# Optimization experiments

Hardware: AMD Instinct MI355X
Metric: run time of the kernel (lower is better)

Reference implementation:

```python
import jax, jax.numpy as jnp
import numpy as np

N_HEAD = 16


def setup_inputs() -> dict:
    key = jax.random.key(0)
    k1, k2, k3 = jax.random.split(key, 3)
    B, T, C = 4, 2048, 1024
    x = jax.random.normal(k1, (B, T, C), dtype=jnp.float32)
    Wqkv = jax.random.normal(k2, (C, 3 * C), dtype=jnp.float32) * 0.02
    Wproj = jax.random.normal(k3, (C, C), dtype=jnp.float32) * 0.02
    return {"x": x, "Wqkv": Wqkv, "Wproj": Wproj}


def reference(x, Wqkv, Wproj):
    B, T, C = x.shape
    nh = N_HEAD
    hd = C // nh
    qkv = x @ Wqkv                                  # (B, T, 3C)
    q, k, v = jnp.split(qkv, 3, axis=-1)
    # (B, T, C) -> (B, nh, T, hd)
    q = q.reshape(B, T, nh, hd).transpose(0, 2, 1, 3)
    k = k.reshape(B, T, nh, hd).transpose(0, 2, 1, 3)
    v = v.reshape(B, T, nh, hd).transpose(0, 2, 1, 3)
    # scaled dot-product attention with causal mask (past_kv=None => T_all == T)
    att = jnp.einsum("bhtd,bhsd->bhts", q, k) / jnp.sqrt(jnp.float32(hd))
    causal = jnp.tril(jnp.ones((T, T), dtype=bool))  # (T, T)
    att = jnp.where(causal[None, None, :, :], att, jnp.float32(-jnp.inf))
    att = jax.nn.softmax(att, axis=-1)              # (B, nh, T, T)
    y = jnp.einsum("bhts,bhsd->bhtd", att, v)       # (B, nh, T, hd)
    y = y.transpose(0, 2, 1, 3).reshape(B, T, C)
    y = y @ Wproj                                   # (B, T, C)
    # present_kv (detached in original)
    return y, jax.lax.stop_gradient(k), jax.lax.stop_gradient(v)
```

## Files before the change

kernel.cpp:

```cpp
#include <hip/hip_runtime.h>
#include <hip/hip_bf16.h>


typedef __bf16 bf16;
typedef __attribute__((ext_vector_type(8))) __bf16 bf16x8;
typedef __attribute__((ext_vector_type(4))) __bf16 bf16x4;
typedef __attribute__((ext_vector_type(4))) float f32x4;

#define AS_G __attribute__((address_space(1)))
#define AS_L __attribute__((address_space(3)))

#define QSCALE 0.1803368801111204f

__device__ __forceinline__ void gld_lds16(const bf16* g, bf16* l) {
  __builtin_amdgcn_global_load_lds((const AS_G void*)g, (AS_L void*)l, 16, 0, 0);
}

__global__ __launch_bounds__(256) void k_cast(const float* __restrict__ in,
                                              bf16* __restrict__ out, int n) {
  int i = (blockIdx.x * 256 + threadIdx.x) * 8;
  if (i >= n) return;
  float4 a = *(const float4*)(in + i);
  float4 b = *(const float4*)(in + i + 4);
  bf16x8 o;
  o[0] = (bf16)a.x; o[1] = (bf16)a.y; o[2] = (bf16)a.z; o[3] = (bf16)a.w;
  o[4] = (bf16)b.x; o[5] = (bf16)b.y; o[6] = (bf16)b.z; o[7] = (bf16)b.w;
  *(bf16x8*)(out + i) = o;
}

__global__ __launch_bounds__(256) void k_transpose(const float* __restrict__ in,
                                                   bf16* __restrict__ out,
                                                   int K, int N) {
  __shared__ float tile[32][33];
  int bx = blockIdx.x * 32;
  int by = blockIdx.y * 32;
  int tx = threadIdx.x, ty = threadIdx.y;
#pragma unroll
  for (int i = 0; i < 4; ++i)
    tile[ty + i * 8][tx] = in[(size_t)(by + ty + i * 8) * N + bx + tx];
  __syncthreads();
#pragma unroll
  for (int i = 0; i < 4; ++i)
    out[(size_t)(bx + ty + i * 8) * K + by + tx] = (bf16)tile[tx][ty + i * 8];
}

__device__ __forceinline__ void gemm_tile_128(const bf16* __restrict__ A,
                                              const bf16* __restrict__ Bt,
                                              int m0, int n0,
                                              bf16* As, bf16* Bs,
                                              f32x4 acc[4][4]) {
  const int tid = threadIdx.x;
  const int w = tid >> 6, lane = tid & 63, lo = lane & 15, hi = lane >> 4;
  const int wm = w >> 1, wn = w & 1;
#pragma unroll 1
  for (int k0 = 0; k0 < 1024; k0 += 32) {
#pragma unroll
    for (int p = 0; p < 2; ++p) {
      int u = tid + 256 * p;
      int row = u >> 2, cs = u & 3;
      int g = cs ^ ((row >> 1) & 3);
      gld_lds16(A + (size_t)(m0 + row) * 1024 + k0 + g * 8, As + p * 2048 + w * 512);
      gld_lds16(Bt + (size_t)(n0 + row) * 1024 + k0 + g * 8, Bs + p * 2048 + w * 512);
    }
    __syncthreads();
    bf16x8 af[4], bfr[4];
#pragma unroll
    for (int i = 0; i < 4; ++i) {
      int row = wm * 64 + i * 16 + lo;
      af[i] = *(const bf16x8*)(As + row * 32 + (hi ^ ((row >> 1) & 3)) * 8);
    }
#pragma unroll
    for (int j = 0; j < 4; ++j) {
      int row = wn * 64 + j * 16 + lo;
      bfr[j] = *(const bf16x8*)(Bs + row * 32 + (hi ^ ((row >> 1) & 3)) * 8);
    }
#pragma unroll
    for (int i = 0; i < 4; ++i)
#pragma unroll
      for (int j = 0; j < 4; ++j)
        acc[i][j] = __builtin_amdgcn_mfma_f32_16x16x32_bf16(af[i], bfr[j], acc[i][j], 0, 0, 0);
    __syncthreads();
  }
}

__global__ __launch_bounds__(256) void k_gemm_qkv(const bf16* __restrict__ x,
                                                  const bf16* __restrict__ WqkvT,
                                                  bf16* __restrict__ qb, bf16* __restrict__ kb,
                                                  bf16* __restrict__ vtb,
                                                  float* __restrict__ outk, float* __restrict__ outv) {
  __shared__ bf16 As[128 * 32], Bs[128 * 32];
  f32x4 acc[4][4] = {};
  int m0 = blockIdx.y * 128, n0 = blockIdx.x * 128;
  gemm_tile_128(x, WqkvT, m0, n0, As, Bs, acc);
  const int tid = threadIdx.x;
  const int w = tid >> 6, lane = tid & 63, lo = lane & 15, hi = lane >> 4;
  const int wm = w >> 1, wn = w & 1;
#pragma unroll
  for (int i = 0; i < 4; ++i) {
    int growbase = m0 + wm * 64 + i * 16 + hi * 4;
    int b = growbase >> 11, t0 = growbase & 2047;
#pragma unroll
    for (int j = 0; j < 4; ++j) {
      int gcol = n0 + wn * 64 + j * 16 + lo;
      int part = gcol >> 10;
      int cc = gcol & 1023, h = cc >> 6, d = cc & 63;
      size_t idx0 = ((size_t)(b * 16 + h) * 2048 + t0) * 64 + d;
      if (part == 0) {
#pragma unroll
        for (int r = 0; r < 4; ++r) qb[idx0 + (size_t)r * 64] = (bf16)(acc[i][j][r] * QSCALE);
      } else if (part == 1) {
#pragma unroll
        for (int r = 0; r < 4; ++r) {
          float val = acc[i][j][r];
          kb[idx0 + (size_t)r * 64] = (bf16)val;
          outk[idx0 + (size_t)r * 64] = val;
        }
      } else {
        bf16x4 pk;
#pragma unroll
        for (int r = 0; r < 4; ++r) {
          float val = acc[i][j][r];
          outv[idx0 + (size_t)r * 64] = val;
          pk[r] = (bf16)val;
        }
        *(bf16x4*)(vtb + ((size_t)(b * 16 + h) * 64 + d) * 2048 + t0) = pk;
      }
    }
  }
}

__global__ __launch_bounds__(256) void k_gemm_proj(const bf16* __restrict__ yb,
                                                   const bf16* __restrict__ WprojT,
                                                   float* __restrict__ out) {
  __shared__ bf16 As[128 * 32], Bs[128 * 32];
  f32x4 acc[4][4] = {};
  int m0 = blockIdx.y * 128, n0 = blockIdx.x * 128;
  gemm_tile_128(yb, WprojT, m0, n0, As, Bs, acc);
  const int tid = threadIdx.x;
  const int w = tid >> 6, lane = tid & 63, lo = lane & 15, hi = lane >> 4;
  const int wm = w >> 1, wn = w & 1;
#pragma unroll
  for (int i = 0; i < 4; ++i)
#pragma unroll
    for (int j = 0; j < 4; ++j)
#pragma unroll
      for (int r = 0; r < 4; ++r) {
        int grow = m0 + wm * 64 + i * 16 + hi * 4 + r;
        int gcol = n0 + wn * 64 + j * 16 + lo;
        out[(size_t)grow * 1024 + gcol] = acc[i][j][r];
      }
}

__device__ __forceinline__ void p_store(f32x4 sacc[4], bool mask,
                                        int w, int lo, int hi, bf16* psrow) {
  if (mask) {
#pragma unroll
    for (int nt = 0; nt < 4; ++nt)
#pragma unroll
      for (int r = 0; r < 4; ++r)
        if (nt * 16 + hi * 4 + r > w * 16 + lo) sacc[nt][r] = -1e30f;
  }
#pragma unroll
  for (int nt = 0; nt < 4; ++nt) {
    bf16x4 pk;
#pragma unroll
    for (int r = 0; r < 4; ++r) pk[r] = (bf16)exp2f(sacc[nt][r]);
    *(bf16x4*)(psrow + (w * 16 + lo) * 72 + nt * 16 + hi * 4) = pk;
  }
}

__device__ __forceinline__ void write_y(bf16* __restrict__ y, int b, int h, int qrow,
                                        int hi, const f32x4 o[4], float inv) {
  size_t base = ((size_t)b * 2048 + qrow) * 1024 + h * 64;
#pragma unroll
  for (int mt = 0; mt < 4; ++mt) {
    bf16x4 yk;
#pragma unroll
    for (int r = 0; r < 4; ++r) yk[r] = (bf16)(o[mt][r] * inv);
    *(bf16x4*)(y + base + mt * 16 + hi * 4) = yk;
  }
}

__global__ __launch_bounds__(256, 4) void k_flash(const bf16* __restrict__ q,
                                                  const bf16* __restrict__ k,
                                                  const bf16* __restrict__ vt,
                                                  bf16* __restrict__ y) {
  __shared__ bf16 Ks[64 * 64];
  __shared__ bf16 Vs[80 * 64];
  __shared__ bf16 Ps[128 * 72];
  const int bi = blockIdx.x;
  const int slot = bi >> 3;
  const int bh = (bi & 7) + 8 * (slot >> 4);
  const int j = slot & 15;
  const int jA = j, jB = 31 - j;
  const int tid = threadIdx.x, w = tid >> 6, lane = tid & 63, lo = lane & 15, hi = lane >> 4;
  const bf16* qp = q + (size_t)bh * 2048 * 64;
  const bf16* kp = k + (size_t)bh * 2048 * 64;
  const bf16* vtp = vt + (size_t)bh * 64 * 2048;

  {
    int rr = tid >> 4, c = (tid & 15) * 4;
    bf16x4 z;
    bf16 v1 = (rr == 0) ? (bf16)1.0f : (bf16)0.0f;
    z[0] = v1; z[1] = v1; z[2] = v1; z[3] = v1;
    *(bf16x4*)(Vs + (64 + rr) * 64 + c) = z;
  }

  bf16x8 qfA[2], qfB[2];
  {
    int qA = jA * 64 + w * 16 + lo;
    int qB = jB * 64 + w * 16 + lo;
    qfA[0] = *(const bf16x8*)(qp + (size_t)qA * 64 + hi * 8);
    qfA[1] = *(const bf16x8*)(qp + (size_t)qA * 64 + 32 + hi * 8);
    qfB[0] = *(const bf16x8*)(qp + (size_t)qB * 64 + hi * 8);
    qfB[1] = *(const bf16x8*)(qp + (size_t)qB * 64 + 32 + hi * 8);
  }
  f32x4 oA[4] = {}, oB[4] = {};
  f32x4 oLA = {}, oLB = {};

  for (int st = 0; st <= jB; ++st) {
    const int s0 = st * 64;
#pragma unroll
    for (int p = 0; p < 2; ++p) {
      int u = tid + 256 * p;
      int row = u >> 3, c = u & 7, g = c ^ (row & 7);
      gld_lds16(kp + (size_t)(s0 + row) * 64 + g * 8, Ks + p * 2048 + w * 512);
      gld_lds16(vtp + (size_t)row * 2048 + s0 + g * 8, Vs + p * 2048 + w * 512);
    }
    __syncthreads();

    bf16x8 kf[4][2];
#pragma unroll
    for (int nt = 0; nt < 4; ++nt)
#pragma unroll
      for (int ks = 0; ks < 2; ++ks)
        kf[nt][ks] = *(const bf16x8*)(Ks + (nt * 16 + lo) * 64 + ((ks * 4 + hi) ^ (lo & 7)) * 8);

    const bool actA = (st <= jA);
    if (actA) {
      f32x4 sacc[4] = {};
#pragma unroll
      for (int nt = 0; nt < 4; ++nt)
#pragma unroll
        for (int ks = 0; ks < 2; ++ks)
          sacc[nt] = __builtin_amdgcn_mfma_f32_16x16x32_bf16(kf[nt][ks], qfA[ks], sacc[nt], 0, 0, 0);
      p_store(sacc, st == jA, w, lo, hi, Ps);
    }
    {
      f32x4 sacc[4] = {};
#pragma unroll
      for (int nt = 0; nt < 4; ++nt)
#pragma unroll
        for (int ks = 0; ks < 2; ++ks)
          sacc[nt] = __builtin_amdgcn_mfma_f32_16x16x32_bf16(kf[nt][ks], qfB[ks], sacc[nt], 0, 0, 0);
      p_store(sacc, st == jB, w, lo, hi, Ps + 64 * 72);
    }
    __asm__ volatile("s_waitcnt lgkmcnt(0)" ::: "memory");

    bf16x8 pfA[2], pfB[2];
#pragma unroll
    for (int ks = 0; ks < 2; ++ks) {
      pfB[ks] = *(const bf16x8*)(Ps + (64 + w * 16 + lo) * 72 + ks * 32 + hi * 8);
      if (actA) pfA[ks] = *(const bf16x8*)(Ps + (w * 16 + lo) * 72 + ks * 32 + hi * 8);
    }
#pragma unroll
    for (int mt = 0; mt < 5; ++mt) {
#pragma unroll
      for (int ks = 0; ks < 2; ++ks) {
        int row = mt * 16 + lo;
        bf16x8 vf = *(const bf16x8*)(Vs + row * 64 + ((ks * 4 + hi) ^ (row & 7)) * 8);
        if (mt < 4) {
          oB[mt] = __builtin_amdgcn_mfma_f32_16x16x32_bf16(vf, pfB[ks], oB[mt], 0, 0, 0);
          if (actA) oA[mt] = __builtin_amdgcn_mfma_f32_16x16x32_bf16(vf, pfA[ks], oA[mt], 0, 0, 0);
        } else {
          oLB = __builtin_amdgcn_mfma_f32_16x16x32_bf16(vf, pfB[ks], oLB, 0, 0, 0);
          if (actA) oLA = __builtin_amdgcn_mfma_f32_16x16x32_bf16(vf, pfA[ks], oLA, 0, 0, 0);
        }
      }
    }
    __syncthreads();
  }

  const int b = bh >> 4, h = bh & 15;
  float lA = __shfl(oLA[0], lo, 64);
  float lB = __shfl(oLB[0], lo, 64);
  write_y(y, b, h, jA * 64 + w * 16 + lo, hi, oA, 1.0f / lA);
  write_y(y, b, h, jB * 64 + w * 16 + lo, hi, oB, 1.0f / lB);
}

extern "C" void kernel_launch(void* const* d_in, const int* in_sizes, int n_in,
                              void* d_out, int out_size, void* d_ws, size_t ws_size,
                              hipStream_t stream) {
  const float* x = (const float*)d_in[0];
  const float* Wqkv = (const float*)d_in[1];
  const float* Wproj = (const float*)d_in[2];
  float* out = (float*)d_out;

  const size_t YSZ = (size_t)8192 * 1024;
  char* ws = (char*)d_ws;
  bf16* xb = (bf16*)ws;      ws += (size_t)8192 * 1024 * 2;
  bf16* wqkvT = (bf16*)ws;   ws += (size_t)3072 * 1024 * 2;
  bf16* wprojT = (bf16*)ws;  ws += (size_t)1024 * 1024 * 2;
  bf16* qb = (bf16*)ws;      ws += (size_t)64 * 2048 * 64 * 2;
  bf16* kb = (bf16*)ws;      ws += (size_t)64 * 2048 * 64 * 2;
  bf16* vtb = (bf16*)ws;     ws += (size_t)64 * 2048 * 64 * 2;
  bf16* yb = (bf16*)ws;

  float* outy = out;
  float* outk = out + YSZ;
  float* outv = out + 2 * YSZ;

  k_cast<<<4096, 256, 0, stream>>>(x, xb, 8388608);
  dim3 tb(32, 8);
  k_transpose<<<dim3(96, 32), tb, 0, stream>>>(Wqkv, wqkvT, 1024, 3072);
  k_transpose<<<dim3(32, 32), tb, 0, stream>>>(Wproj, wprojT, 1024, 1024);
  k_gemm_qkv<<<dim3(24, 64), 256, 0, stream>>>(xb, wqkvT, qb, kb, vtb, outk, outv);
  k_flash<<<1024, 256, 0, stream>>>(qb, kb, vtb, yb);
  k_gemm_proj<<<dim3(8, 64), 256, 0, stream>>>(yb, wprojT, outy);
}
```

Baseline: 324.3 us.

## Rewrite GEMMs as 256x128 tiles with triple-buffered async LDS pipeline

Replaces the simple 128x128 GEMM tile (K-step 32, load then sync each step) with a 256x128 tile using 512 threads. The new loop takes a K-step of 64, keeps three LDS buffers with direct global-to-LDS loads issued two steps ahead and vmcnt waits, and interleaves fragment loads with MFMA phases under s_setprio. Blocks are remapped through an XCD-aware swizzle of a 1D grid so neighbouring tiles share L2. The aim is to hide global load latency and raise MFMA utilisation, at the cost of much more LDS (144KB per block) and fragile manual barrier and waitcnt logic.

New measurement: 309.0 us. 4.7% less time.

```diff
diff --git a/kernel.cpp b/kernel.cpp
--- a/kernel.cpp
+++ b/kernel.cpp
@@ -44,74 +44,158 @@
     out[(size_t)(bx + ty + i * 8) * K + by + tx] = (bf16)tile[tx][ty + i * 8];
 }
 
-__device__ __forceinline__ void gemm_tile_128(const bf16* __restrict__ A,
-                                              const bf16* __restrict__ Bt,
-                                              int m0, int n0,
-                                              bf16* As, bf16* Bs,
-                                              f32x4 acc[4][4]) {
+__device__ __forceinline__ void gemm_main_256x128(const bf16* __restrict__ A,
+                                                  const bf16* __restrict__ Bt,
+                                                  int m0, int n0,
+                                                  bf16* As, bf16* Bs,
+                                                  f32x4 acc[4][4]) {
   const int tid = threadIdx.x;
   const int w = tid >> 6, lane = tid & 63, lo = lane & 15, hi = lane >> 4;
   const int wm = w >> 1, wn = w & 1;
+  const int urow = tid >> 3;
+  const int gsw = (tid & 7) ^ (urow & 7);
+  const bf16* ga = A + (size_t)(m0 + urow) * 1024 + gsw * 8;
+  const bf16* gb = Bt + (size_t)(n0 + urow) * 1024 + gsw * 8;
+  const int p0 = hi ^ (lo & 7);
+  const int aRow = wm * 64 + lo;
+  const int bRow = wn * 64 + lo;
+
+#define STAGE_A2(t, bufi, s0) do {                                                              \
+    gld_lds16(ga + (size_t)(s0) * 65536 + (t) * 64,                                             \
+              As + (bufi) * 16384 + (s0) * 4096 + w * 512);                                     \
+    gld_lds16(ga + (size_t)((s0) + 1) * 65536 + (t) * 64,                                       \
+              As + (bufi) * 16384 + ((s0) + 1) * 4096 + w * 512);                               \
+  } while (0)
+#define STAGE_B2(t, bufi) do {                                                                  \
+    gld_lds16(gb + (t) * 64, Bs + (bufi) * 8192 + w * 512);                                     \
+    gld_lds16(gb + 65536 + (t) * 64, Bs + (bufi) * 8192 + 4096 + w * 512);                      \
+  } while (0)
+
+  STAGE_A2(0, 0, 0); STAGE_A2(0, 0, 2); STAGE_B2(0, 0);
+  STAGE_A2(1, 1, 0); STAGE_A2(1, 1, 2); STAGE_B2(1, 1);
+
+  bf16x8 a[2][2], b[4][2];
+  int buf = 0, sbuf = 2;
 #pragma unroll 1
-  for (int k0 = 0; k0 < 1024; k0 += 32) {
-#pragma unroll
-    for (int p = 0; p < 2; ++p) {
-      int u = tid + 256 * p;
-      int row = u >> 2, cs = u & 3;
-      int g = cs ^ ((row >> 1) & 3);
-      gld_lds16(A + (size_t)(m0 + row) * 1024 + k0 + g * 8, As + p * 2048 + w * 512);
-      gld_lds16(Bt + (size_t)(n0 + row) * 1024 + k0 + g * 8, Bs + p * 2048 + w * 512);
-    }
-    __syncthreads();
-    bf16x8 af[4], bfr[4];
-#pragma unroll
-    for (int i = 0; i < 4; ++i) {
-      int row = wm * 64 + i * 16 + lo;
-      af[i] = *(const bf16x8*)(As + row * 32 + (hi ^ ((row >> 1) & 3)) * 8);
-    }
-#pragma unroll
-    for (int j = 0; j < 4; ++j) {
-      int row = wn * 64 + j * 16 + lo;
-      bfr[j] = *(const bf16x8*)(Bs + row * 32 + (hi ^ ((row >> 1) & 3)) * 8);
-    }
-#pragma unroll
-    for (int i = 0; i < 4; ++i)
-#pragma unroll
-      for (int j = 0; j < 4; ++j)
-        acc[i][j] = __builtin_amdgcn_mfma_f32_16x16x32_bf16(af[i], bfr[j], acc[i][j], 0, 0, 0);
-    __syncthreads();
-  }
-}
-
-__global__ __launch_bounds__(256) void k_gemm_qkv(const bf16* __restrict__ x,
-                                                  const bf16* __restrict__ WqkvT,
-                                                  bf16* __restrict__ qb, bf16* __restrict__ kb,
-                                                  bf16* __restrict__ vtb,
-                                                  float* __restrict__ outk, float* __restrict__ outv) {
-  __shared__ bf16 As[128 * 32], Bs[128 * 32];
+  for (int t = 0; t < 16; ++t) {
+    if (t < 15) asm volatile("s_waitcnt vmcnt(6)" ::: "memory");
+    else        asm volatile("s_waitcnt vmcnt(0)" ::: "memory");
+    __builtin_amdgcn_s_barrier();
+    const bf16* Ab = As + buf * 16384;
+    const bf16* Bb = Bs + buf * 8192;
+
+#pragma unroll
+    for (int mi = 0; mi < 2; ++mi) {
+      const bf16* r = Ab + (aRow + mi * 16) * 64;
+      a[mi][0] = *(const bf16x8*)(r + p0 * 8);
+      a[mi][1] = *(const bf16x8*)(r + (p0 ^ 4) * 8);
+    }
+#pragma unroll
+    for (int ni = 0; ni < 2; ++ni) {
+      const bf16* r = Bb + (bRow + ni * 16) * 64;
+      b[ni][0] = *(const bf16x8*)(r + p0 * 8);
+      b[ni][1] = *(const bf16x8*)(r + (p0 ^ 4) * 8);
+    }
+    if (t < 14) STAGE_A2(t + 2, sbuf, 0);
+    __builtin_amdgcn_s_barrier();
+    __builtin_amdgcn_s_setprio(1);
+#pragma unroll
+    for (int ks = 0; ks < 2; ++ks)
+#pragma unroll
+      for (int mi = 0; mi < 2; ++mi)
+#pragma unroll
+        for (int ni = 0; ni < 2; ++ni)
+          acc[mi][ni] = __builtin_amdgcn_mfma_f32_16x16x32_bf16(a[mi][ks], b[ni][ks], acc[mi][ni], 0, 0, 0);
+    __builtin_amdgcn_s_setprio(0);
+    __builtin_amdgcn_s_barrier();
+
+#pragma unroll
+    for (int ni = 0; ni < 2; ++ni) {
+      const bf16* r = Bb + (bRow + (ni + 2) * 16) * 64;
+      b[ni + 2][0] = *(const bf16x8*)(r + p0 * 8);
+      b[ni + 2][1] = *(const bf16x8*)(r + (p0 ^ 4) * 8);
+    }
+    if (t < 14) STAGE_A2(t + 2, sbuf, 2);
+    __builtin_amdgcn_s_barrier();
+    __builtin_amdgcn_s_setprio(1);
+#pragma unroll
+    for (int ks = 0; ks < 2; ++ks)
+#pragma unroll
+      for (int mi = 0; mi < 2; ++mi)
+#pragma unroll
+        for (int ni = 0; ni < 2; ++ni)
+          acc[mi][ni + 2] = __builtin_amdgcn_mfma_f32_16x16x32_bf16(a[mi][ks], b[ni + 2][ks], acc[mi][ni + 2], 0, 0, 0);
+    __builtin_amdgcn_s_setprio(0);
+    __builtin_amdgcn_s_barrier();
+
+#pragma unroll
+    for (int mi = 0; mi < 2; ++mi) {
+      const bf16* r = Ab + (aRow + (mi + 2) * 16) * 64;
+      a[mi][0] = *(const bf16x8*)(r + p0 * 8);
+      a[mi][1] = *(const bf16x8*)(r + (p0 ^ 4) * 8);
+    }
+    if (t < 14) STAGE_B2(t + 2, sbuf);
+    __builtin_amdgcn_s_barrier();
+    __builtin_amdgcn_s_setprio(1);
+#pragma unroll
+    for (int ks = 0; ks < 2; ++ks)
+#pragma unroll
+      for (int mi = 0; mi < 2; ++mi)
+#pragma unroll
+        for (int ni = 0; ni < 2; ++ni)
+          acc[mi + 2][ni + 2] = __builtin_amdgcn_mfma_f32_16x16x32_bf16(a[mi][ks], b[ni + 2][ks], acc[mi + 2][ni + 2], 0, 0, 0);
+    __builtin_amdgcn_s_setprio(0);
+    __builtin_amdgcn_s_barrier();
+
+    __builtin_amdgcn_s_setprio(1);
+#pragma unroll
+    for (int ks = 0; ks < 2; ++ks)
+#pragma unroll
+      for (int mi = 0; mi < 2; ++mi)
+#pragma unroll
+        for (int ni = 0; ni < 2; ++ni)
+          acc[mi + 2][ni] = __builtin_amdgcn_mfma_f32_16x16x32_bf16(a[mi][ks], b[ni][ks], acc[mi + 2][ni], 0, 0, 0);
+    __builtin_amdgcn_s_setprio(0);
+
+    buf = (buf == 2) ? 0 : buf + 1;
+    sbuf = (sbuf == 2) ? 0 : sbuf + 1;
+  }
+#undef STAGE_A2
+#undef STAGE_B2
+}
+
+__global__ __launch_bounds__(512, 2) void k_gemm_qkv(const bf16* __restrict__ x,
+                                                     const bf16* __restrict__ WqkvT,
+                                                     bf16* __restrict__ qb, bf16* __restrict__ kb,
+                                                     bf16* __restrict__ vtb,
+                                                     float* __restrict__ outk, float* __restrict__ outv) {
+  __shared__ bf16 As[49152], Bs[24576];
+  int id = blockIdx.x;
+  int swz = (id & 7) * 96 + (id >> 3);
+  int by = swz / 24, bx = swz - by * 24;
+  int m0 = by * 256, n0 = bx * 128;
   f32x4 acc[4][4] = {};
-  int m0 = blockIdx.y * 128, n0 = blockIdx.x * 128;
-  gemm_tile_128(x, WqkvT, m0, n0, As, Bs, acc);
+  gemm_main_256x128(x, WqkvT, m0, n0, As, Bs, acc);
   const int tid = threadIdx.x;
   const int w = tid >> 6, lane = tid & 63, lo = lane & 15, hi = lane >> 4;
   const int wm = w >> 1, wn = w & 1;
 #pragma unroll
-  for (int i = 0; i < 4; ++i) {
-    int growbase = m0 + wm * 64 + i * 16 + hi * 4;
-    int b = growbase >> 11, t0 = growbase & 2047;
-#pragma unroll
-    for (int j = 0; j < 4; ++j) {
-      int gcol = n0 + wn * 64 + j * 16 + lo;
+  for (int mi = 0; mi < 4; ++mi) {
+    int growbase = m0 + wm * 64 + mi * 16 + hi * 4;
+    int bb = growbase >> 11, t0 = growbase & 2047;
+#pragma unroll
+    for (int ni = 0; ni < 4; ++ni) {
+      int gcol = n0 + wn * 64 + ni * 16 + lo;
       int part = gcol >> 10;
       int cc = gcol & 1023, h = cc >> 6, d = cc & 63;
-      size_t idx0 = ((size_t)(b * 16 + h) * 2048 + t0) * 64 + d;
+      size_t idx0 = ((size_t)(bb * 16 + h) * 2048 + t0) * 64 + d;
       if (part == 0) {
 #pragma unroll
-        for (int r = 0; r < 4; ++r) qb[idx0 + (size_t)r * 64] = (bf16)(acc[i][j][r] * QSCALE);
+        for (int r = 0; r < 4; ++r) qb[idx0 + (size_t)r * 64] = (bf16)(acc[mi][ni][r] * QSCALE);
       } else if (part == 1) {
 #pragma unroll
         for (int r = 0; r < 4; ++r) {
-          float val = acc[i][j][r];
+          float val = acc[mi][ni][r];
           kb[idx0 + (size_t)r * 64] = (bf16)val;
           outk[idx0 + (size_t)r * 64] = val;
         }
@@ -119,35 +203,38 @@
         bf16x4 pk;
 #pragma unroll
         for (int r = 0; r < 4; ++r) {
-          float val = acc[i][j][r];
+          float val = acc[mi][ni][r];
           outv[idx0 + (size_t)r * 64] = val;
           pk[r] = (bf16)val;
         }
-        *(bf16x4*)(vtb + ((size_t)(b * 16 + h) * 64 + d) * 2048 + t0) = pk;
+        *(bf16x4*)(vtb + ((size_t)(bb * 16 + h) * 64 + d) * 2048 + t0) = pk;
       }
     }
   }
 }
 
-__global__ __launch_bounds__(256) void k_gemm_proj(const bf16* __restrict__ yb,
-                                                   const bf16* __restrict__ WprojT,
-                                                   float* __restrict__ out) {
-  __shared__ bf16 As[128 * 32], Bs[128 * 32];
+__global__ __launch_bounds__(512, 2) void k_gemm_proj(const bf16* __restrict__ yb,
+                                                      const bf16* __restrict__ WprojT,
+                                                      float* __restrict__ out) {
+  __shared__ bf16 As[49152], Bs[24576];
+  int id = blockIdx.x;
+  int swz = (id & 7) * 32 + (id >> 3);
+  int by = swz >> 3, bx = swz & 7;
+  int m0 = by * 256, n0 = bx * 128;
   f32x4 acc[4][4] = {};
-  int m0 = blockIdx.y * 128, n0 = blockIdx.x * 128;
-  gemm_tile_128(yb, WprojT, m0, n0, As, Bs, acc);
+  gemm_main_256x128(yb, WprojT, m0, n0, As, Bs, acc);
   const int tid = threadIdx.x;
   const int w = tid >> 6, lane = tid & 63, lo = lane & 15, hi = lane >> 4;
   const int wm = w >> 1, wn = w & 1;
 #pragma unroll
-  for (int i = 0; i < 4; ++i)
-#pragma unroll
-    for (int j = 0; j < 4; ++j)
+  for (int mi = 0; mi < 4; ++mi)
+#pragma unroll
+    for (int ni = 0; ni < 4; ++ni)
 #pragma unroll
       for (int r = 0; r < 4; ++r) {
-        int grow = m0 + wm * 64 + i * 16 + hi * 4 + r;
-        int gcol = n0 + wn * 64 + j * 16 + lo;
-        out[(size_t)grow * 1024 + gcol] = acc[i][j][r];
+        int grow = m0 + wm * 64 + mi * 16 + hi * 4 + r;
+        int gcol = n0 + wn * 64 + ni * 16 + lo;
+        out[(size_t)grow * 1024 + gcol] = acc[mi][ni][r];
       }
 }
 
@@ -314,7 +401,7 @@
   dim3 tb(32, 8);
   k_transpose<<<dim3(96, 32), tb, 0, stream>>>(Wqkv, wqkvT, 1024, 3072);
   k_transpose<<<dim3(32, 32), tb, 0, stream>>>(Wproj, wprojT, 1024, 1024);
-  k_gemm_qkv<<<dim3(24, 64), 256, 0, stream>>>(xb, wqkvT, qb, kb, vtb, outk, outv);
+  k_gemm_qkv<<<768, 512, 0, stream>>>(xb, wqkvT, qb, kb, vtb, outk, outv);
   k_flash<<<1024, 256, 0, stream>>>(qb, kb, vtb, yb);
-  k_gemm_proj<<<dim3(8, 64), 256, 0, stream>>>(yb, wprojT, outy);
-}
+  k_gemm_proj<<<256, 512, 0, stream>>>(yb, wprojT, outy);
+}
```
